# Performance work log

Hardware: AMD Instinct MI355X
Metric: run time of the kernel (lower is better)

Reference implementation:

```python
import jax, jax.numpy as jnp
import numpy as np

N_NODES = 200000
N_EDGES = 3200000
NUM_GRAPHS = 100
WIN = 30
H1, H2, OUT = 500, 20, 4


def setup_inputs() -> dict:
    key = jax.random.key(0)
    ks = jax.random.split(key, 8)
    features = jax.random.normal(ks[0], (N_NODES, WIN), dtype=jnp.float32)
    src = jax.random.randint(ks[1], (N_EDGES,), 0, N_NODES, dtype=jnp.int32)
    dst = jax.random.randint(ks[2], (N_EDGES,), 0, N_NODES, dtype=jnp.int32)
    # contiguous equal-size graphs: 2000 nodes per graph -> ids sorted 0..99
    graph_ids = (jnp.arange(N_NODES, dtype=jnp.int32) // (N_NODES // NUM_GRAPHS))
    W1 = jax.random.normal(ks[3], (WIN, H1), dtype=jnp.float32) / np.sqrt(WIN)
    b1 = jnp.zeros((H1,), jnp.float32)
    W2 = jax.random.normal(ks[4], (H1, H2), dtype=jnp.float32) / np.sqrt(H1)
    b2 = jnp.zeros((H2,), jnp.float32)
    W3 = jax.random.normal(ks[5], (H2, OUT), dtype=jnp.float32) / np.sqrt(H2)
    b3 = jnp.zeros((OUT,), jnp.float32)
    return {"features": features, "src": src, "dst": dst, "graph_ids": graph_ids,
            "num_graphs": NUM_GRAPHS, "W1": W1, "b1": b1, "W2": W2, "b2": b2,
            "W3": W3, "b3": b3}


def reference(features, src, dst, graph_ids, num_graphs, W1, b1, W2, b2, W3, b3):
    N = features.shape[0]
    ones = jnp.ones(src.shape[0], dtype=features.dtype)
    # DGL GraphConv norm='both': D_out^{-1/2} on src side, D_in^{-1/2} on dst side
    deg_out = jnp.maximum(jax.ops.segment_sum(ones, src, num_segments=N), 1.0)
    deg_in = jnp.maximum(jax.ops.segment_sum(ones, dst, num_segments=N), 1.0)
    x = features * jax.lax.rsqrt(deg_out)[:, None]
    # aggregate first (in_feats < out_feats), then dense transform
    agg = jax.ops.segment_sum(x[src], dst, num_segments=N)          # [N, 30]
    agg = agg * jax.lax.rsqrt(deg_in)[:, None]
    h = jax.nn.silu(agg @ W1 + b1)                                   # [N, 500]
    pooled = jax.ops.segment_max(h, graph_ids, num_segments=num_graphs)  # [G, 500]
    y = jax.nn.silu(pooled @ W2 + b2)                                # dropout = identity (eval)
    return jax.nn.sigmoid(y @ W3 + b3)                               # [G, 4]
```

## Files before the change

kernel.cpp:

```cpp
#include <hip/hip_runtime.h>
#include <hip/hip_fp16.h>

#define WIN 30
#define H1 500
#define H1P 512
#define H2 20
#define OUTD 4
#define CS 4
#define NBIN 61440
#define NBINW (NBIN/4)
#define NCH 48
#define RPB 512
#define MAXPB 9216
#define BINCHUNK 8192
#define NBMAX 400

typedef _Float16 f16x8 __attribute__((ext_vector_type(8)));
typedef float f32x4 __attribute__((ext_vector_type(4)));

__global__ __launch_bounds__(512) void k_hist(const int* __restrict__ src,
                                              unsigned* __restrict__ partial,
                                              int* __restrict__ gcur,
                                              int E, int NB) {
    __shared__ unsigned h[NBINW];
    const int tid = threadIdx.x;
    if (blockIdx.x == 0)
        for (int j = tid; j < NB; j += 512) gcur[j] = 0;
    const int r = blockIdx.x / NCH, c = blockIdx.x % NCH;
    const int base = r * NBIN;
    for (int j = tid; j < NBINW; j += 512) h[j] = 0;
    __syncthreads();
    const int ce = ((E + NCH - 1) / NCH + 3) & ~3;
    const int start = c * ce;
    const int end = min(E, start + ce);
    for (int i = start + tid * 4; i < end; i += 512 * 4) {
        if (i + 3 < end) {
            int4 s4 = *(const int4*)(src + i);
            unsigned d;
            d = (unsigned)(s4.x - base); if (d < NBIN) atomicAdd(&h[d >> 2], 1u << ((d & 3) * 8));
            d = (unsigned)(s4.y - base); if (d < NBIN) atomicAdd(&h[d >> 2], 1u << ((d & 3) * 8));
            d = (unsigned)(s4.z - base); if (d < NBIN) atomicAdd(&h[d >> 2], 1u << ((d & 3) * 8));
            d = (unsigned)(s4.w - base); if (d < NBIN) atomicAdd(&h[d >> 2], 1u << ((d & 3) * 8));
        } else {
            for (int k = i; k < end; ++k) {
                unsigned d = (unsigned)(src[k] - base);
                if (d < NBIN) atomicAdd(&h[d >> 2], 1u << ((d & 3) * 8));
            }
        }
    }
    __syncthreads();
    unsigned* outp = partial + (size_t)blockIdx.x * NBINW;
    for (int j = tid; j < NBINW; j += 512) outp[j] = h[j];
}

__global__ __launch_bounds__(256) void k_prep2(const unsigned* __restrict__ partial,
                                               const float* __restrict__ feat,
                                               const float* __restrict__ W1,
                                               __half* __restrict__ xh,
                                               __half* __restrict__ w1cm,
                                               int N, int nmb) {
    const int tid = threadIdx.x;
    if (blockIdx.x == nmb) {
        for (int i = tid; i < H1P * 32; i += 256) {
            int c = i >> 5, k = i & 31;
            float v = (k < WIN && c < H1) ? W1[k * H1 + c] : 0.f;
            w1cm[i] = __float2half(v);
        }
        return;
    }
    __shared__ float rs[1024];
    {
        int w = blockIdx.x * 256 + tid;
        int node0 = 4 * w;
        int r = node0 / NBIN;
        int lw = (node0 - r * NBIN) >> 2;
        const unsigned* p = partial + (size_t)(r * NCH) * NBINW + lw;
        unsigned b0 = 0, b1 = 0, b2 = 0, b3 = 0;
        for (int c = 0; c < NCH; ++c) {
            unsigned v = p[(size_t)c * NBINW];
            b0 += v & 0xFFu; b1 += (v >> 8) & 0xFFu;
            b2 += (v >> 16) & 0xFFu; b3 += v >> 24;
        }
        rs[tid * 4 + 0] = rsqrtf((float)max((int)b0, 1));
        rs[tid * 4 + 1] = rsqrtf((float)max((int)b1, 1));
        rs[tid * 4 + 2] = rsqrtf((float)max((int)b2, 1));
        rs[tid * 4 + 3] = rsqrtf((float)max((int)b3, 1));
    }
    __syncthreads();
    const int nbase = blockIdx.x * 1024;
    for (int task = tid; task < 1024 * 4; task += 256) {
        int node_l = task >> 2;
        int node = nbase + node_l;
        if (node >= N) break;
        int c8 = (task & 3) * 8;
        float r = rs[node_l];
        float f[8];
#pragma unroll
        for (int q = 0; q < 8; ++q) {
            int d = c8 + q;
            f[q] = (d < WIN) ? feat[(size_t)node * WIN + d] * r : 0.f;
        }
        union { uint4 u4; __half2 h2[4]; } y;
        y.h2[0] = __floats2half2_rn(f[0], f[1]);
        y.h2[1] = __floats2half2_rn(f[2], f[3]);
        y.h2[2] = __floats2half2_rn(f[4], f[5]);
        y.h2[3] = __floats2half2_rn(f[6], f[7]);
        *(uint4*)(xh + (size_t)node * 32 + c8) = y.u4;
    }
}

__global__ __launch_bounds__(1024) void k_bin(const int* __restrict__ src,
                                              const int* __restrict__ dst,
                                              int* __restrict__ gcur,
                                              unsigned* __restrict__ ebuf,
                                              int E, int NB) {
    __shared__ int cnt[NBMAX];
    __shared__ int base[NBMAX];
    const int tid = threadIdx.x;
    for (int j = tid; j < NB; j += 1024) cnt[j] = 0;
    __syncthreads();
    const int start = blockIdx.x * BINCHUNK;
    const int end = min(E, start + BINCHUNK);
    for (int i = start + tid; i < end; i += 1024)
        atomicAdd(&cnt[dst[i] >> 9], 1);
    __syncthreads();
    for (int j = tid; j < NB; j += 1024) {
        int c = cnt[j];
        base[j] = j * MAXPB + (c ? atomicAdd(&gcur[j], c) : 0);
        cnt[j] = 0;
    }
    __syncthreads();
    for (int i = start + tid; i < end; i += 1024) {
        int d = dst[i];
        int b = d >> 9;
        int idx = atomicAdd(&cnt[b], 1);
        int pos = base[b] + idx;
        if (pos < (b + 1) * MAXPB)
            ebuf[pos] = ((unsigned)src[i] << 9) | (unsigned)(d & 511);
    }
}

__global__ __launch_bounds__(1024) void k_agg(const __half* __restrict__ xh,
                                              const unsigned* __restrict__ ebuf,
                                              const int* __restrict__ gcur,
                                              __half* __restrict__ agg, int N) {
    __shared__ unsigned es[MAXPB];
    __shared__ int cnt[RPB + 1];
    __shared__ int cur[RPB];
    const int tid = threadIdx.x;
    const int b = blockIdx.x;
    for (int j = tid; j < RPB; j += 1024) { cnt[j + 1] = 0; cur[j] = 0; }
    if (tid == 0) cnt[0] = 0;
    __syncthreads();
    const int ne = min(gcur[b], MAXPB);
    const unsigned* eb = ebuf + (size_t)b * MAXPB;
    for (int i = tid; i < ne; i += 1024)
        atomicAdd(&cnt[(int)(eb[i] & (RPB - 1)) + 1], 1);
    __syncthreads();
    if (tid < 64) {
        const int i0 = tid * 8;
        int s[8];
        int run = 0;
#pragma unroll
        for (int k = 0; k < 8; ++k) { run += cnt[i0 + k + 1]; s[k] = run; }
        int inc = run;
#pragma unroll
        for (int o = 1; o < 64; o <<= 1) {
            int u = __shfl_up(inc, o, 64);
            if (tid >= o) inc += u;
        }
        const int ex = inc - run;
#pragma unroll
        for (int k = 0; k < 8; ++k) cnt[i0 + k + 1] = ex + s[k];
    }
    __syncthreads();
    for (int i = tid; i < ne; i += 1024) {
        unsigned p = eb[i];
        int ld = (int)(p & (RPB - 1));
        int idx = atomicAdd(&cur[ld], 1);
        es[cnt[ld] + idx] = p;
    }
    __syncthreads();
    for (int task = tid; task < RPB * 4; task += 1024) {
        const int node_l = task >> 2;
        const int c8 = (task & 3) * 8;
        const int o0 = cnt[node_l], o1 = cnt[node_l + 1];
        float a0 = 0.f, a1 = 0.f, a2 = 0.f, a3 = 0.f;
        float a4 = 0.f, a5 = 0.f, a6 = 0.f, a7 = 0.f;
        int j = o0;
        for (; j + 3 < o1; j += 4) {
            unsigned p0 = es[j], p1 = es[j + 1], p2 = es[j + 2], p3 = es[j + 3];
            union { uint4 u4; __half2 h2[4]; } x0, x1, x2, x3;
            x0.u4 = *(const uint4*)(xh + (size_t)(p0 >> 9) * 32 + c8);
            x1.u4 = *(const uint4*)(xh + (size_t)(p1 >> 9) * 32 + c8);
            x2.u4 = *(const uint4*)(xh + (size_t)(p2 >> 9) * 32 + c8);
            x3.u4 = *(const uint4*)(xh + (size_t)(p3 >> 9) * 32 + c8);
            a0 += __low2float(x0.h2[0]) + __low2float(x1.h2[0]) + __low2float(x2.h2[0]) + __low2float(x3.h2[0]);
            a1 += __high2float(x0.h2[0]) + __high2float(x1.h2[0]) + __high2float(x2.h2[0]) + __high2float(x3.h2[0]);
            a2 += __low2float(x0.h2[1]) + __low2float(x1.h2[1]) + __low2float(x2.h2[1]) + __low2float(x3.h2[1]);
            a3 += __high2float(x0.h2[1]) + __high2float(x1.h2[1]) + __high2float(x2.h2[1]) + __high2float(x3.h2[1]);
            a4 += __low2float(x0.h2[2]) + __low2float(x1.h2[2]) + __low2float(x2.h2[2]) + __low2float(x3.h2[2]);
            a5 += __high2float(x0.h2[2]) + __high2float(x1.h2[2]) + __high2float(x2.h2[2]) + __high2float(x3.h2[2]);
            a6 += __low2float(x0.h2[3]) + __low2float(x1.h2[3]) + __low2float(x2.h2[3]) + __low2float(x3.h2[3]);
            a7 += __high2float(x0.h2[3]) + __high2float(x1.h2[3]) + __high2float(x2.h2[3]) + __high2float(x3.h2[3]);
        }
        for (; j < o1; ++j) {
            unsigned p0 = es[j];
            union { uint4 u4; __half2 h2[4]; } x0;
            x0.u4 = *(const uint4*)(xh + (size_t)(p0 >> 9) * 32 + c8);
            a0 += __low2float(x0.h2[0]);  a1 += __high2float(x0.h2[0]);
            a2 += __low2float(x0.h2[1]);  a3 += __high2float(x0.h2[1]);
            a4 += __low2float(x0.h2[2]);  a5 += __high2float(x0.h2[2]);
            a6 += __low2float(x0.h2[3]);  a7 += __high2float(x0.h2[3]);
        }
        const int node = b * RPB + node_l;
        if (node < N) {
            float deg = (float)(o1 - o0);
            float r = rsqrtf(fmaxf(deg, 1.f));
            union { uint4 u4; __half2 h2[4]; } y;
            y.h2[0] = __floats2half2_rn(a0 * r, a1 * r);
            y.h2[1] = __floats2half2_rn(a2 * r, a3 * r);
            y.h2[2] = __floats2half2_rn(a4 * r, a5 * r);
            y.h2[3] = __floats2half2_rn(a6 * r, a7 * r);
            *(uint4*)(agg + (size_t)node * 32 + c8) = y.u4;
        }
    }
}

__global__ __launch_bounds__(256) void k_gemm(const __half* __restrict__ agg,
                                              const __half* __restrict__ w1cm,
                                              const float* __restrict__ b1,
                                              float* __restrict__ pooled,
                                              int NPG, int G) {
    const int bid = blockIdx.x;
    const int g = bid / CS, c = bid % CS;
    const int tid = threadIdx.x;
    const int w = tid >> 6;
    const int l = tid & 63;
    const int lo = l & 15, hi = l >> 4;

    f16x8 bfr[8];
#pragma unroll
    for (int ct = 0; ct < 8; ++ct) {
        int col = c * 128 + ct * 16 + lo;
        bfr[ct] = *(const f16x8*)(w1cm + (size_t)col * 32 + hi * 8);
    }
    float vmax[8], vmin[8];
#pragma unroll
    for (int ct = 0; ct < 8; ++ct) { vmax[ct] = -INFINITY; vmin[ct] = INFINITY; }

    const int mts = NPG >> 4;
    for (int mt = w; mt < mts; mt += 4) {
        int node = g * NPG + mt * 16 + lo;
        f16x8 a = *(const f16x8*)(agg + (size_t)node * 32 + hi * 8);
#pragma unroll
        for (int ct = 0; ct < 8; ++ct) {
            f32x4 acc = {0.f, 0.f, 0.f, 0.f};
            acc = __builtin_amdgcn_mfma_f32_16x16x32_f16(a, bfr[ct], acc, 0, 0, 0);
#pragma unroll
            for (int q = 0; q < 4; ++q) {
                vmax[ct] = fmaxf(vmax[ct], acc[q]);
                vmin[ct] = fminf(vmin[ct], acc[q]);
            }
        }
    }
#pragma unroll
    for (int ct = 0; ct < 8; ++ct) {
        vmax[ct] = fmaxf(vmax[ct], __shfl_xor(vmax[ct], 16, 64));
        vmax[ct] = fmaxf(vmax[ct], __shfl_xor(vmax[ct], 32, 64));
        vmin[ct] = fminf(vmin[ct], __shfl_xor(vmin[ct], 16, 64));
        vmin[ct] = fminf(vmin[ct], __shfl_xor(vmin[ct], 32, 64));
    }
    __shared__ float red[2][4][8][16];
    if (hi == 0) {
#pragma unroll
        for (int ct = 0; ct < 8; ++ct) {
            red[0][w][ct][lo] = vmax[ct];
            red[1][w][ct][lo] = vmin[ct];
        }
    }
    __syncthreads();
    if (tid < 128) {
        int ct = tid >> 4, col16 = tid & 15;
        float m = fmaxf(fmaxf(red[0][0][ct][col16], red[0][1][ct][col16]),
                        fmaxf(red[0][2][ct][col16], red[0][3][ct][col16]));
        float n = fminf(fminf(red[1][0][ct][col16], red[1][1][ct][col16]),
                        fminf(red[1][2][ct][col16], red[1][3][ct][col16]));
        int col = c * 128 + ct * 16 + col16;
        float bb = (col < H1) ? b1[col] : 0.f;
        m += bb; n += bb;
        float sm = m / (1.f + __expf(-m));
        float sn = n / (1.f + __expf(-n));
        pooled[(size_t)g * H1P + col] = fmaxf(sm, sn);
    }
}

__global__ __launch_bounds__(64) void k_head(const float* __restrict__ pooled,
                                             const float* __restrict__ W2,
                                             const float* __restrict__ b2,
                                             const float* __restrict__ W3,
                                             const float* __restrict__ b3,
                                             float* __restrict__ out, int G) {
    const int g = blockIdx.x;
    const int t = threadIdx.x;
    __shared__ float y[H2];
    if (t < H2) {
        float acc = b2[t];
        for (int k = 0; k < H1; ++k)
            acc = fmaf(pooled[(size_t)g * H1P + k], W2[k * H2 + t], acc);
        y[t] = acc / (1.f + __expf(-acc));
    }
    __syncthreads();
    if (t < OUTD) {
        float acc = b3[t];
#pragma unroll
        for (int k = 0; k < H2; ++k) acc = fmaf(y[k], W3[k * OUTD + t], acc);
        out[g * OUTD + t] = 1.f / (1.f + __expf(-acc));
    }
}

static inline size_t align256(size_t x) { return (x + 255) & ~(size_t)255; }

extern "C" void kernel_launch(void* const* d_in, const int* in_sizes, int n_in,
                              void* d_out, int out_size, void* d_ws, size_t ws_size,
                              hipStream_t stream) {
    const float* feat = (const float*)d_in[0];
    const int*   src  = (const int*)d_in[1];
    const int*   dst  = (const int*)d_in[2];
    const float* W1 = (const float*)d_in[5];
    const float* b1 = (const float*)d_in[6];
    const float* W2 = (const float*)d_in[7];
    const float* b2 = (const float*)d_in[8];
    const float* W3 = (const float*)d_in[9];
    const float* b3 = (const float*)d_in[10];
    float* out = (float*)d_out;

    const int N = in_sizes[0] / WIN;
    const int E = in_sizes[1];
    const int G = out_size / OUTD;
    const int NPG = N / G;
    const int nr = (N + NBIN - 1) / NBIN;
    const int NB = (N + RPB - 1) / RPB;
    const int nmb = (N + 1023) / 1024;

    char* ws = (char*)d_ws;
    size_t off = 0;
    unsigned* partial = (unsigned*)(ws + off); off += align256((size_t)nr * NCH * NBINW * 4);
    __half*   xh      = (__half*)(ws + off);   off += align256((size_t)N * 32 * 2);
    __half*   w1cm    = (__half*)(ws + off);   off += align256((size_t)H1P * 32 * 2);
    __half*   agg     = (__half*)(ws + off);   off += align256((size_t)N * 32 * 2);
    float*    pooled  = (float*)(ws + off);    off += align256((size_t)G * H1P * 4);
    int*      gcur    = (int*)(ws + off);      off += align256((size_t)NB * 4);
    unsigned* ebuf    = (unsigned*)(ws + off); off += align256((size_t)NB * MAXPB * 4 + 256);
    (void)ws_size; (void)n_in;

    k_hist<<<nr * NCH, 512, 0, stream>>>(src, partial, gcur, E, NB);
    k_prep2<<<nmb + 1, 256, 0, stream>>>(partial, feat, W1, xh, w1cm, N, nmb);
    k_bin<<<(E + BINCHUNK - 1) / BINCHUNK, 1024, 0, stream>>>(src, dst, gcur, ebuf, E, NB);
    k_agg<<<NB, 1024, 0, stream>>>(xh, ebuf, gcur, agg, N);
    k_gemm<<<G * CS, 256, 0, stream>>>(agg, w1cm, b1, pooled, NPG, G);
    k_head<<<G, 64, 0, stream>>>(pooled, W2, b2, W3, b3, out, G);
}
```

Before: 165.8 us.

## Merge histogram and binning kernels, fuse MLP head into GEMM tail

The degree histogram and the dst-binning kernels now run as one launch, with the blocks split by index between the two roles. The counter reset moves to a memset. The MLP head is folded into the pooling GEMM kernel: the last of the CS column blocks for each graph, found through an atomic counter and thread fences, computes the head. This removes two kernel launches and lets the histogram and binning work overlap, at the cost of an extra memset, a larger block size for the histogram part, and fence/atomic overhead in the GEMM.

Measured after the change: 190.7 us. 1.15x slower.

```diff
diff --git a/kernel.cpp b/kernel.cpp
--- a/kernel.cpp
+++ b/kernel.cpp
@@ -18,39 +18,66 @@
 typedef _Float16 f16x8 __attribute__((ext_vector_type(8)));
 typedef float f32x4 __attribute__((ext_vector_type(4)));
 
-__global__ __launch_bounds__(512) void k_hist(const int* __restrict__ src,
-                                              unsigned* __restrict__ partial,
-                                              int* __restrict__ gcur,
-                                              int E, int NB) {
+__global__ __launch_bounds__(1024) void k_hb(const int* __restrict__ src,
+                                             const int* __restrict__ dst,
+                                             unsigned* __restrict__ partial,
+                                             int* __restrict__ gcur,
+                                             unsigned* __restrict__ ebuf,
+                                             int E, int NB, int NHB) {
     __shared__ unsigned h[NBINW];
     const int tid = threadIdx.x;
-    if (blockIdx.x == 0)
-        for (int j = tid; j < NB; j += 512) gcur[j] = 0;
-    const int r = blockIdx.x / NCH, c = blockIdx.x % NCH;
-    const int base = r * NBIN;
-    for (int j = tid; j < NBINW; j += 512) h[j] = 0;
-    __syncthreads();
-    const int ce = ((E + NCH - 1) / NCH + 3) & ~3;
-    const int start = c * ce;
-    const int end = min(E, start + ce);
-    for (int i = start + tid * 4; i < end; i += 512 * 4) {
-        if (i + 3 < end) {
-            int4 s4 = *(const int4*)(src + i);
-            unsigned d;
-            d = (unsigned)(s4.x - base); if (d < NBIN) atomicAdd(&h[d >> 2], 1u << ((d & 3) * 8));
-            d = (unsigned)(s4.y - base); if (d < NBIN) atomicAdd(&h[d >> 2], 1u << ((d & 3) * 8));
-            d = (unsigned)(s4.z - base); if (d < NBIN) atomicAdd(&h[d >> 2], 1u << ((d & 3) * 8));
-            d = (unsigned)(s4.w - base); if (d < NBIN) atomicAdd(&h[d >> 2], 1u << ((d & 3) * 8));
-        } else {
-            for (int k = i; k < end; ++k) {
-                unsigned d = (unsigned)(src[k] - base);
-                if (d < NBIN) atomicAdd(&h[d >> 2], 1u << ((d & 3) * 8));
+    if ((int)blockIdx.x < NHB) {
+        const int r = blockIdx.x / NCH, c = blockIdx.x % NCH;
+        const int nbase = r * NBIN;
+        for (int j = tid; j < NBINW; j += 1024) h[j] = 0;
+        __syncthreads();
+        const int ce = ((E + NCH - 1) / NCH + 3) & ~3;
+        const int start = c * ce;
+        const int end = min(E, start + ce);
+        for (int i = start + tid * 4; i < end; i += 1024 * 4) {
+            if (i + 3 < end) {
+                int4 s4 = *(const int4*)(src + i);
+                unsigned d;
+                d = (unsigned)(s4.x - nbase); if (d < NBIN) atomicAdd(&h[d >> 2], 1u << ((d & 3) * 8));
+                d = (unsigned)(s4.y - nbase); if (d < NBIN) atomicAdd(&h[d >> 2], 1u << ((d & 3) * 8));
+                d = (unsigned)(s4.z - nbase); if (d < NBIN) atomicAdd(&h[d >> 2], 1u << ((d & 3) * 8));
+                d = (unsigned)(s4.w - nbase); if (d < NBIN) atomicAdd(&h[d >> 2], 1u << ((d & 3) * 8));
+            } else {
+                for (int k = i; k < end; ++k) {
+                    unsigned d = (unsigned)(src[k] - nbase);
+                    if (d < NBIN) atomicAdd(&h[d >> 2], 1u << ((d & 3) * 8));
+                }
             }
         }
-    }
-    __syncthreads();
-    unsigned* outp = partial + (size_t)blockIdx.x * NBINW;
-    for (int j = tid; j < NBINW; j += 512) outp[j] = h[j];
+        __syncthreads();
+        unsigned* outp = partial + (size_t)blockIdx.x * NBINW;
+        for (int j = tid; j < NBINW; j += 1024) outp[j] = h[j];
+    } else {
+        int* cnt = (int*)h;
+        int* base = (int*)h + NBMAX;
+        const int bb = blockIdx.x - NHB;
+        for (int j = tid; j < NB; j += 1024) cnt[j] = 0;
+        __syncthreads();
+        const int start = bb * BINCHUNK;
+        const int end = min(E, start + BINCHUNK);
+        for (int i = start + tid; i < end; i += 1024)
+            atomicAdd(&cnt[dst[i] >> 9], 1);
+        __syncthreads();
+        for (int j = tid; j < NB; j += 1024) {
+            int c = cnt[j];
+            base[j] = j * MAXPB + (c ? atomicAdd(&gcur[j], c) : 0);
+            cnt[j] = 0;
+        }
+        __syncthreads();
+        for (int i = start + tid; i < end; i += 1024) {
+            int d = dst[i];
+            int b = d >> 9;
+            int idx = atomicAdd(&cnt[b], 1);
+            int pos = base[b] + idx;
+            if (pos < (b + 1) * MAXPB)
+                ebuf[pos] = ((unsigned)src[i] << 9) | (unsigned)(d & 511);
+        }
+    }
 }
 
 __global__ __launch_bounds__(256) void k_prep2(const unsigned* __restrict__ partial,
@@ -60,7 +87,7 @@
                                                __half* __restrict__ w1cm,
                                                int N, int nmb) {
     const int tid = threadIdx.x;
-    if (blockIdx.x == nmb) {
+    if ((int)blockIdx.x == nmb) {
         for (int i = tid; i < H1P * 32; i += 256) {
             int c = i >> 5, k = i & 31;
             float v = (k < WIN && c < H1) ? W1[k * H1 + c] : 0.f;
@@ -106,37 +133,6 @@
         y.h2[2] = __floats2half2_rn(f[4], f[5]);
         y.h2[3] = __floats2half2_rn(f[6], f[7]);
         *(uint4*)(xh + (size_t)node * 32 + c8) = y.u4;
-    }
-}
-
-__global__ __launch_bounds__(1024) void k_bin(const int* __restrict__ src,
-                                              const int* __restrict__ dst,
-                                              int* __restrict__ gcur,
-                                              unsigned* __restrict__ ebuf,
-                                              int E, int NB) {
-    __shared__ int cnt[NBMAX];
-    __shared__ int base[NBMAX];
-    const int tid = threadIdx.x;
-    for (int j = tid; j < NB; j += 1024) cnt[j] = 0;
-    __syncthreads();
-    const int start = blockIdx.x * BINCHUNK;
-    const int end = min(E, start + BINCHUNK);
-    for (int i = start + tid; i < end; i += 1024)
-        atomicAdd(&cnt[dst[i] >> 9], 1);
-    __syncthreads();
-    for (int j = tid; j < NB; j += 1024) {
-        int c = cnt[j];
-        base[j] = j * MAXPB + (c ? atomicAdd(&gcur[j], c) : 0);
-        cnt[j] = 0;
-    }
-    __syncthreads();
-    for (int i = start + tid; i < end; i += 1024) {
-        int d = dst[i];
-        int b = d >> 9;
-        int idx = atomicAdd(&cnt[b], 1);
-        int pos = base[b] + idx;
-        if (pos < (b + 1) * MAXPB)
-            ebuf[pos] = ((unsigned)src[i] << 9) | (unsigned)(d & 511);
     }
 }
 
@@ -230,7 +226,13 @@
 __global__ __launch_bounds__(256) void k_gemm(const __half* __restrict__ agg,
                                               const __half* __restrict__ w1cm,
                                               const float* __restrict__ b1,
+                                              const float* __restrict__ W2,
+                                              const float* __restrict__ b2,
+                                              const float* __restrict__ W3,
+                                              const float* __restrict__ b3,
                                               float* __restrict__ pooled,
+                                              int* __restrict__ gcnt,
+                                              float* __restrict__ out,
                                               int NPG, int G) {
     const int bid = blockIdx.x;
     const int g = bid / CS, c = bid % CS;
@@ -293,29 +295,27 @@
         float sn = n / (1.f + __expf(-n));
         pooled[(size_t)g * H1P + col] = fmaxf(sm, sn);
     }
-}
-
-__global__ __launch_bounds__(64) void k_head(const float* __restrict__ pooled,
-                                             const float* __restrict__ W2,
-                                             const float* __restrict__ b2,
-                                             const float* __restrict__ W3,
-                                             const float* __restrict__ b3,
-                                             float* __restrict__ out, int G) {
-    const int g = blockIdx.x;
-    const int t = threadIdx.x;
+    __shared__ bool last;
     __shared__ float y[H2];
-    if (t < H2) {
-        float acc = b2[t];
-        for (int k = 0; k < H1; ++k)
-            acc = fmaf(pooled[(size_t)g * H1P + k], W2[k * H2 + t], acc);
-        y[t] = acc / (1.f + __expf(-acc));
-    }
-    __syncthreads();
-    if (t < OUTD) {
-        float acc = b3[t];
-#pragma unroll
-        for (int k = 0; k < H2; ++k) acc = fmaf(y[k], W3[k * OUTD + t], acc);
-        out[g * OUTD + t] = 1.f / (1.f + __expf(-acc));
+    __threadfence();
+    __syncthreads();
+    if (tid == 0) last = (atomicAdd(&gcnt[g], 1) == CS - 1);
+    __syncthreads();
+    if (last) {
+        __threadfence();
+        if (tid < H2) {
+            float acc = b2[tid];
+            for (int k = 0; k < H1; ++k)
+                acc = fmaf(pooled[(size_t)g * H1P + k], W2[k * H2 + tid], acc);
+            y[tid] = acc / (1.f + __expf(-acc));
+        }
+        __syncthreads();
+        if (tid < OUTD) {
+            float acc = b3[tid];
+#pragma unroll
+            for (int k = 0; k < H2; ++k) acc = fmaf(y[k], W3[k * OUTD + tid], acc);
+            out[g * OUTD + tid] = 1.f / (1.f + __expf(-acc));
+        }
     }
 }
 
@@ -340,7 +340,9 @@
     const int G = out_size / OUTD;
     const int NPG = N / G;
     const int nr = (N + NBIN - 1) / NBIN;
+    const int NHB = nr * NCH;
     const int NB = (N + RPB - 1) / RPB;
+    const int NBB = (E + BINCHUNK - 1) / BINCHUNK;
     const int nmb = (N + 1023) / 1024;
 
     char* ws = (char*)d_ws;
@@ -350,14 +352,15 @@
     __half*   w1cm    = (__half*)(ws + off);   off += align256((size_t)H1P * 32 * 2);
     __half*   agg     = (__half*)(ws + off);   off += align256((size_t)N * 32 * 2);
     float*    pooled  = (float*)(ws + off);    off += align256((size_t)G * H1P * 4);
-    int*      gcur    = (int*)(ws + off);      off += align256((size_t)NB * 4);
+    int*      gcur    = (int*)(ws + off);      off += align256((size_t)(NB + G) * 4);
+    int*      gcnt    = gcur + NB;
     unsigned* ebuf    = (unsigned*)(ws + off); off += align256((size_t)NB * MAXPB * 4 + 256);
     (void)ws_size; (void)n_in;
 
-    k_hist<<<nr * NCH, 512, 0, stream>>>(src, partial, gcur, E, NB);
+    hipMemsetAsync(gcur, 0, (size_t)(NB + G) * 4, stream);
+    k_hb<<<NHB + NBB, 1024, 0, stream>>>(src, dst, partial, gcur, ebuf, E, NB, NHB);
     k_prep2<<<nmb + 1, 256, 0, stream>>>(partial, feat, W1, xh, w1cm, N, nmb);
-    k_bin<<<(E + BINCHUNK - 1) / BINCHUNK, 1024, 0, stream>>>(src, dst, gcur, ebuf, E, NB);
     k_agg<<<NB, 1024, 0, stream>>>(xh, ebuf, gcur, agg, N);
-    k_gemm<<<G * CS, 256, 0, stream>>>(agg, w1cm, b1, pooled, NPG, G);
-    k_head<<<G, 64, 0, stream>>>(pooled, W2, b2, W3, b3, out, G);
-}
+    k_gemm<<<G * CS, 256, 0, stream>>>(agg, w1cm, b1, W2, b2, W3, b3,
+                                       pooled, gcnt, out, NPG, G);
+}
```
